# Performance work log

Measured on AMD Instinct MI355X. Metric: run time of the kernel, lower is better.

## Reference

```python
import jax, jax.numpy as jnp
import numpy as np

B, S, D, H, L = 4, 2048, 512, 8, 4
DFF = 4 * D
CW = 128          # context_window
LS_MIN, LS_MAX = -6.0, 1.5


def setup_inputs() -> dict:
    key = jax.random.key(0)
    ks = jax.random.split(key, 10)
    s = 0.02
    p = lambda k, shape: jax.random.normal(k, shape, jnp.float32) * s
    return {
        "x": jax.random.normal(ks[0], (B, S, 2), jnp.float32),
        "W_in": p(ks[1], (D, 2)), "b_in": jnp.zeros((D,), jnp.float32),
        "pos": p(ks[2], (1, S, D)),
        "Wqkv": p(ks[3], (L, 3 * D, D)), "bqkv": jnp.zeros((L, 3 * D), jnp.float32),
        "Wo": p(ks[4], (L, D, D)), "bo": jnp.zeros((L, D), jnp.float32),
        "W1": p(ks[5], (L, DFF, D)), "b1": jnp.zeros((L, DFF), jnp.float32),
        "W2": p(ks[6], (L, D, DFF)), "b2": jnp.zeros((L, D), jnp.float32),
        "ln1_g": jnp.ones((L, D), jnp.float32), "ln1_b": jnp.zeros((L, D), jnp.float32),
        "ln2_g": jnp.ones((L, D), jnp.float32), "ln2_b": jnp.zeros((L, D), jnp.float32),
        "W_head": p(ks[7], (4, D)), "b_head": jnp.zeros((4,), jnp.float32),
    }


def _ln(x, g, b):
    m = x.mean(-1, keepdims=True)
    v = ((x - m) ** 2).mean(-1, keepdims=True)
    return (x - m) / jnp.sqrt(v + 1e-5) * g + b


def reference(x, W_in, b_in, pos, Wqkv, bqkv, Wo, bo, W1, b1, W2, b2,
              ln1_g, ln1_b, ln2_g, ln2_b, W_head, b_head):
    Bx, Sx, _ = x.shape
    h = x @ W_in.T + b_in + pos[:, :Sx, :]          # [B,S,D]
    idx = jnp.arange(Sx)
    # True = disallowed: future OR older than context window
    mask = (idx[None, :] > idx[:, None]) | (idx[None, :] < idx[:, None] - CW)
    dh = D // H
    scale = 1.0 / np.sqrt(dh).astype(np.float32)
    neg = jnp.float32(-1e30)
    for l in range(L):
        # self-attention (post-LN, as nn.TransformerEncoderLayer default)
        qkv = h @ Wqkv[l].T + bqkv[l]               # [B,S,3D]
        q, k, v = jnp.split(qkv, 3, axis=-1)
        q = q.reshape(Bx, Sx, H, dh)
        k = k.reshape(Bx, Sx, H, dh)
        v = v.reshape(Bx, Sx, H, dh)
        scores = jnp.einsum('bqhd,bkhd->bhqk', q, k) * scale
        scores = jnp.where(mask, neg, scores)
        attn = jax.nn.softmax(scores, axis=-1)
        o = jnp.einsum('bhqk,bkhd->bqhd', attn, v).reshape(Bx, Sx, D)
        h = _ln(h + o @ Wo[l].T + bo[l], ln1_g[l], ln1_b[l])
        # GELU FFN (exact erf gelu, torch default)
        ff = jax.nn.gelu(h @ W1[l].T + b1[l], approximate=False) @ W2[l].T + b2[l]
        h = _ln(h + ff, ln2_g[l], ln2_b[l])
    out = h @ W_head.T + b_head                     # [B,S,4]
    mu = out[..., :2]
    log_sigma = jnp.clip(out[..., 2:], LS_MIN, LS_MAX)
    return mu, log_sigma
```

## Files before the change

kernel.cpp:

```cpp
#include <hip/hip_runtime.h>
#include <hip/hip_bf16.h>
#include <math.h>

constexpr int Bc = 4;
constexpr int Sc = 2048;
constexpr int Dc = 512;
constexpr int Hc = 8;
constexpr int DHc = 64;
constexpr int Lc = 4;
constexpr int DFFc = 2048;
constexpr int Tc = Bc * Sc;
constexpr int QKVW = 3 * Dc;

typedef __attribute__((ext_vector_type(8))) short short8;
typedef __attribute__((ext_vector_type(4))) float f32x4;
typedef __attribute__((ext_vector_type(4))) float float4v;
typedef __attribute__((ext_vector_type(4))) unsigned int uint4v;

static __device__ __forceinline__ float u16tof(unsigned int u) {
  return __uint_as_float(u << 16);
}
static __device__ __forceinline__ unsigned short ftobf(float f) {
  __hip_bfloat16 h = __float2bfloat16(f);
  return *reinterpret_cast<unsigned short*>(&h);
}
static __device__ __forceinline__ void gload_lds16(const void* g, void* l) {
  __builtin_amdgcn_global_load_lds(
      (const __attribute__((address_space(1))) void*)g,
      (__attribute__((address_space(3))) void*)l, 16, 0, 0);
}

static __device__ __forceinline__ int swzK(int row, int col) {
  return row * 64 + ((((col >> 3) ^ (row & 7)) << 3) | (col & 7));
}
static __device__ __forceinline__ int swzW(int row, int col) {
  return row * 192 + ((((col >> 3) ^ (row & 7)) << 3) | (col & 7));
}

__global__ __launch_bounds__(256) void k_f2bf(const float* __restrict__ in,
                                              unsigned short* __restrict__ out,
                                              int n) {
  int i = blockIdx.x * 256 + threadIdx.x;
  if (i < n) out[i] = ftobf(in[i]);
}

__global__ __launch_bounds__(256) void k_embed(const float* __restrict__ x,
                                               const float* __restrict__ W_in,
                                               const float* __restrict__ b_in,
                                               const float* __restrict__ pos,
                                               float* __restrict__ h,
                                               unsigned short* __restrict__ hb) {
  int idx = blockIdx.x * 256 + threadIdx.x;
  int t = idx >> 9;
  int d = idx & 511;
  int s = t & (Sc - 1);
  float v = x[t * 2 + 0] * W_in[d * 2 + 0] + x[t * 2 + 1] * W_in[d * 2 + 1] +
            b_in[d] + pos[(size_t)s * Dc + d];
  h[idx] = v;
  hb[idx] = ftobf(v);
}

template <int MODE, int OUTBF>
__global__ __launch_bounds__(256, 4) void k_mgemm(const unsigned short* __restrict__ A,
                                                  const unsigned short* __restrict__ W,
                                                  const float* __restrict__ bias,
                                                  void* __restrict__ Cout,
                                                  int M, int N, int K) {
  __shared__ short SMEM[2][2][512 * 8];
  const int tid = threadIdx.x;
  const int lane = tid & 63;
  const int wid = tid >> 6;
  const int wm = wid >> 1;
  const int wn = wid & 1;

  const int nwg = gridDim.x * gridDim.y;
  const int bid = blockIdx.y * gridDim.x + blockIdx.x;
  const int swz = (bid & 7) * (nwg >> 3) + (bid >> 3);
  const int m0 = (swz / gridDim.x) * 128;
  const int n0 = (swz % gridDim.x) * 128;

  int r0S, c0S, r1S, c1S;
  {
    int p = tid;
    int rp = p >> 3, q = (p & 7) ^ (rp & 7);
    r0S = (rp << 1) | (q >> 2);
    c0S = q & 3;
    p = tid + 256;
    rp = p >> 3;
    q = (p & 7) ^ (rp & 7);
    r1S = (rp << 1) | (q >> 2);
    c1S = q & 3;
  }
  const unsigned short* a0p = A + (size_t)(m0 + r0S) * K + c0S * 8;
  const unsigned short* a1p = A + (size_t)(m0 + r1S) * K + c1S * 8;
  const unsigned short* b0p = W + (size_t)(n0 + r0S) * K + c0S * 8;
  const unsigned short* b1p = W + (size_t)(n0 + r1S) * K + c1S * 8;
  const int d0 = (tid & ~63) * 8;
  const int d1 = ((tid + 256) & ~63) * 8;

  f32x4 acc[4][4] = {};
  const int lr = lane & 15;
  const int chr = lane >> 4;

  gload_lds16(a0p, &SMEM[0][0][d0]);
  gload_lds16(a1p, &SMEM[0][0][d1]);
  gload_lds16(b0p, &SMEM[1][0][d0]);
  gload_lds16(b1p, &SMEM[1][0][d1]);
  __syncthreads();

  const int nsteps = K >> 5;
  int buf = 0;
  for (int s = 0; s < nsteps; ++s) {
    if (s + 1 < nsteps) {
      const int ko = (s + 1) << 5;
      gload_lds16(a0p + ko, &SMEM[0][buf ^ 1][d0]);
      gload_lds16(a1p + ko, &SMEM[0][buf ^ 1][d1]);
      gload_lds16(b0p + ko, &SMEM[1][buf ^ 1][d0]);
      gload_lds16(b1p + ko, &SMEM[1][buf ^ 1][d1]);
    }
    short8 af[4], bfr[4];
#pragma unroll
    for (int mi = 0; mi < 4; ++mi) {
      int row = wm * 64 + mi * 16 + lr;
      int rp = row >> 1;
      int p = rp * 8 + (((((row & 1) << 2) | chr)) ^ (rp & 7));
      af[mi] = *(const short8*)&SMEM[0][buf][p * 8];
    }
#pragma unroll
    for (int ni = 0; ni < 4; ++ni) {
      int row = wn * 64 + ni * 16 + lr;
      int rp = row >> 1;
      int p = rp * 8 + (((((row & 1) << 2) | chr)) ^ (rp & 7));
      bfr[ni] = *(const short8*)&SMEM[1][buf][p * 8];
    }
#pragma unroll
    for (int mi = 0; mi < 4; ++mi)
#pragma unroll
      for (int ni = 0; ni < 4; ++ni)
        acc[mi][ni] = __builtin_amdgcn_mfma_f32_16x16x32_bf16(
            af[mi], bfr[ni], acc[mi][ni], 0, 0, 0);
    __syncthreads();
    buf ^= 1;
  }

  float* cw = (float*)&SMEM[0][0][0] + wid * (16 * 68);
  const int cj = lane & 15;
  const int rj4 = (lane >> 4) * 4;
  const int rrd = lane >> 3;
  const int crd = (lane & 7) * 8;
#pragma unroll
  for (int mi = 0; mi < 4; ++mi) {
#pragma unroll
    for (int ni = 0; ni < 4; ++ni) {
      float bn = bias[n0 + wn * 64 + ni * 16 + cj];
#pragma unroll
      for (int j = 0; j < 4; ++j) {
        float v = acc[mi][ni][j] + bn;
        if (MODE == 2) v = 0.5f * v * (1.0f + erff(v * 0.70710678118654752f));
        cw[(rj4 + j) * 68 + ni * 16 + cj] = v;
      }
    }
    __builtin_amdgcn_sched_barrier(0);
#pragma unroll
    for (int t = 0; t < 2; ++t) {
      int rl = t * 8 + rrd;
      float4v v0 = *(const float4v*)&cw[rl * 68 + crd];
      float4v v1 = *(const float4v*)&cw[rl * 68 + crd + 4];
      size_t gbase = (size_t)(m0 + wm * 64 + mi * 16 + rl) * N +
                     (n0 + wn * 64 + crd);
      if (OUTBF) {
        unsigned int w0 = ftobf(v0[0]) | ((unsigned int)ftobf(v0[1]) << 16);
        unsigned int w1 = ftobf(v0[2]) | ((unsigned int)ftobf(v0[3]) << 16);
        unsigned int w2 = ftobf(v1[0]) | ((unsigned int)ftobf(v1[1]) << 16);
        unsigned int w3 = ftobf(v1[2]) | ((unsigned int)ftobf(v1[3]) << 16);
        uint4v pk = {w0, w1, w2, w3};
        *(uint4v*)&((unsigned short*)Cout)[gbase] = pk;
      } else {
        *(float4v*)&((float*)Cout)[gbase] = v0;
        *(float4v*)&((float*)Cout)[gbase + 4] = v1;
      }
    }
    __builtin_amdgcn_sched_barrier(0);
  }
}

__global__ __launch_bounds__(256, 3) void k_attn(const unsigned short* __restrict__ qkv,
                                                 unsigned short* __restrict__ o) {
  __shared__ unsigned short KPs[192 * 64];
  __shared__ unsigned short Vt[64 * 192];

  const int tid = threadIdx.x;
  const int lane = tid & 63;
  const int w = tid >> 6;
  const int idx = blockIdx.x;
  const int qb = idx & 31;
  const int hh = (idx >> 5) & 7;
  const int b = idx >> 8;
  const int q0 = qb * 64;
  const int kstart = max(0, q0 - 128);
  const int nk = q0 + 64 - kstart;

  for (int c = tid; c < nk * 8; c += 256) {
    int j = c >> 3, ch = c & 7;
    short8 kv = *(const short8*)&qkv[(size_t)(b * Sc + kstart + j) * QKVW + Dc + hh * DHc + ch * 8];
    *(short8*)&KPs[swzK(j, ch * 8)] = kv;
  }
  for (int c = tid; c < (nk >> 1) * 8; c += 256) {
    int jp = c >> 3, ch = c & 7;
    int j = jp * 2;
    const unsigned short* base =
        &qkv[(size_t)(b * Sc + kstart + j) * QKVW + 2 * Dc + hh * DHc + ch * 8];
    short8 v0 = *(const short8*)base;
    short8 v1 = *(const short8*)(base + QKVW);
#pragma unroll
    for (int i = 0; i < 8; ++i) {
      unsigned int pk = (unsigned short)v0[i] | ((unsigned int)(unsigned short)v1[i] << 16);
      *(unsigned int*)&Vt[swzW(ch * 8 + i, j)] = pk;
    }
  }
  if (nk < 192) {
    for (int c = tid; c < 64 * 64; c += 256) {
      int d = c >> 6, jo = c & 63;
      *(unsigned int*)&Vt[swzW(d, 64 + jo * 2)] = 0;
    }
  }

  const int qg = q0 + w * 16 + (lane & 15);
  const int kg8 = (lane >> 4) * 8;
  const unsigned short* qp = &qkv[(size_t)(b * Sc + qg) * QKVW + hh * DHc + kg8];
  short8 bq0 = *(const short8*)qp;
  short8 bq1 = *(const short8*)(qp + 32);
  __syncthreads();

  const int jb = max(0, q0 + w * 16 - 128) - kstart;

  f32x4 sacc[9];
#pragma unroll
  for (int t = 0; t < 9; ++t) {
    int key = jb + t * 16 + (lane & 15);
    short8 a0 = *(const short8*)&KPs[swzK(key, kg8)];
    short8 a1 = *(const short8*)&KPs[swzK(key, 32 + kg8)];
    f32x4 z = {0.f, 0.f, 0.f, 0.f};
    z = __builtin_amdgcn_mfma_f32_16x16x32_bf16(a0, bq0, z, 0, 0, 0);
    sacc[t] = __builtin_amdgcn_mfma_f32_16x16x32_bf16(a1, bq1, z, 0, 0, 0);
  }

  const int rj = (lane >> 4) * 4;
  float mx = -1e30f;
#pragma unroll
  for (int t = 0; t < 9; ++t) {
#pragma unroll
    for (int j = 0; j < 4; ++j) {
      int kglob = kstart + jb + t * 16 + rj + j;
      bool valid = (kglob <= qg) && (kglob + 128 >= qg);
      float s = valid ? sacc[t][j] * 0.125f : -1e30f;
      sacc[t][j] = s;
      mx = fmaxf(mx, s);
    }
  }
  mx = fmaxf(mx, __shfl_xor(mx, 16));
  mx = fmaxf(mx, __shfl_xor(mx, 32));
  float sum = 0.f;
#pragma unroll
  for (int t = 0; t < 9; ++t)
#pragma unroll
    for (int j = 0; j < 4; ++j) {
      float e = __expf(sacc[t][j] - mx);
      sacc[t][j] = e;
      sum += e;
    }
  sum += __shfl_xor(sum, 16);
  sum += __shfl_xor(sum, 32);
  const float inv = 1.0f / sum;

  __syncthreads();

  const int prow = w * 16 + (lane & 15);
#pragma unroll
  for (int t = 0; t < 9; ++t) {
    int c0 = jb + t * 16 + rj;
    unsigned int p0 = ftobf(sacc[t][0] * inv) |
                      ((unsigned int)ftobf(sacc[t][1] * inv) << 16);
    unsigned int p1 = ftobf(sacc[t][2] * inv) |
                      ((unsigned int)ftobf(sacc[t][3] * inv) << 16);
    *(unsigned int*)&KPs[swzW(prow, c0)] = p0;
    *(unsigned int*)&KPs[swzW(prow, c0 + 2)] = p1;
  }
  {
    int g2 = (lane >> 4) * 2;
    for (int col = g2; col < jb; col += 8)
      *(unsigned int*)&KPs[swzW(prow, col)] = 0;
    for (int col = jb + 144 + g2; col < 192; col += 8)
      *(unsigned int*)&KPs[swzW(prow, col)] = 0;
  }
  f32x4 oacc[4] = {};
#pragma unroll
  for (int kb = 0; kb < 6; ++kb) {
    short8 pa = *(const short8*)&KPs[swzW(prow, kb * 32 + kg8)];
#pragma unroll
    for (int dt = 0; dt < 4; ++dt) {
      short8 vb = *(const short8*)&Vt[swzW(dt * 16 + (lane & 15), kb * 32 + kg8)];
      oacc[dt] = __builtin_amdgcn_mfma_f32_16x16x32_bf16(pa, vb, oacc[dt], 0, 0, 0);
    }
  }
  const int cj = lane & 15;
#pragma unroll
  for (int j = 0; j < 4; ++j)
#pragma unroll
    for (int dt = 0; dt < 4; ++dt)
      o[(size_t)(b * Sc + q0 + w * 16 + rj + j) * Dc + hh * DHc + dt * 16 + cj] =
          ftobf(oacc[dt][j]);
}

__global__ __launch_bounds__(256) void k_lnr(float* __restrict__ h,
                                             const float* __restrict__ raw,
                                             const float* __restrict__ g,
                                             const float* __restrict__ bta,
                                             unsigned short* __restrict__ outb) {
  const int wid = threadIdx.x >> 6;
  const int lane = threadIdx.x & 63;
  const int t = blockIdx.x * 4 + wid;
  const float4v* hrow = (const float4v*)(h + (size_t)t * Dc);
  const float4v* rrow = (const float4v*)(raw + (size_t)t * Dc);
  float4v v[2];
  float sum = 0.0f, sq = 0.0f;
#pragma unroll
  for (int i = 0; i < 2; ++i) {
    float4v hv = hrow[lane + i * 64];
    float4v rv = rrow[lane + i * 64];
#pragma unroll
    for (int c = 0; c < 4; ++c) {
      float xv = rv[c] + hv[c];
      v[i][c] = xv;
      sum += xv;
      sq += xv * xv;
    }
  }
#pragma unroll
  for (int off = 32; off; off >>= 1) {
    sum += __shfl_xor(sum, off);
    sq += __shfl_xor(sq, off);
  }
  float m = sum * (1.0f / 512.0f);
  float var = sq * (1.0f / 512.0f) - m * m;
  float rstd = rsqrtf(var + 1e-5f);
  float4v* orow = (float4v*)(h + (size_t)t * Dc);
  unsigned int* brow = (unsigned int*)(outb + (size_t)t * Dc);
#pragma unroll
  for (int i = 0; i < 2; ++i) {
    int d4 = (lane + i * 64) * 4;
    float4v ov;
#pragma unroll
    for (int c = 0; c < 4; ++c)
      ov[c] = (v[i][c] - m) * rstd * g[d4 + c] + bta[d4 + c];
    orow[lane + i * 64] = ov;
    unsigned int p0 = ftobf(ov[0]) | ((unsigned int)ftobf(ov[1]) << 16);
    unsigned int p1 = ftobf(ov[2]) | ((unsigned int)ftobf(ov[3]) << 16);
    brow[(lane + i * 64) * 2] = p0;
    brow[(lane + i * 64) * 2 + 1] = p1;
  }
}

__global__ __launch_bounds__(256) void k_head(const float* __restrict__ h,
                                              const float* __restrict__ Wh,
                                              const float* __restrict__ bh,
                                              float* __restrict__ outp) {
  const int wid = threadIdx.x >> 6;
  const int lane = threadIdx.x & 63;
  const int t = blockIdx.x * 4 + wid;
  const float* row = h + (size_t)t * Dc;
  float a0 = 0, a1 = 0, a2 = 0, a3 = 0;
#pragma unroll
  for (int i = 0; i < 8; ++i) {
    int d = lane + i * 64;
    float xv = row[d];
    a0 += xv * Wh[0 * Dc + d];
    a1 += xv * Wh[1 * Dc + d];
    a2 += xv * Wh[2 * Dc + d];
    a3 += xv * Wh[3 * Dc + d];
  }
#pragma unroll
  for (int off = 32; off; off >>= 1) {
    a0 += __shfl_xor(a0, off);
    a1 += __shfl_xor(a1, off);
    a2 += __shfl_xor(a2, off);
    a3 += __shfl_xor(a3, off);
  }
  if (lane == 0) {
    outp[(size_t)t * 2 + 0] = a0 + bh[0];
    outp[(size_t)t * 2 + 1] = a1 + bh[1];
    outp[(size_t)Tc * 2 + (size_t)t * 2 + 0] = fminf(fmaxf(a2 + bh[2], -6.0f), 1.5f);
    outp[(size_t)Tc * 2 + (size_t)t * 2 + 1] = fminf(fmaxf(a3 + bh[3], -6.0f), 1.5f);
  }
}

extern "C" void kernel_launch(void* const* d_in, const int* in_sizes, int n_in,
                              void* d_out, int out_size, void* d_ws, size_t ws_size,
                              hipStream_t stream) {
  const float* x    = (const float*)d_in[0];
  const float* W_in = (const float*)d_in[1];
  const float* b_in = (const float*)d_in[2];
  const float* pos  = (const float*)d_in[3];
  const float* Wqkv = (const float*)d_in[4];
  const float* bqkv = (const float*)d_in[5];
  const float* Wo   = (const float*)d_in[6];
  const float* bo   = (const float*)d_in[7];
  const float* W1   = (const float*)d_in[8];
  const float* b1   = (const float*)d_in[9];
  const float* W2   = (const float*)d_in[10];
  const float* b2   = (const float*)d_in[11];
  const float* ln1g = (const float*)d_in[12];
  const float* ln1b = (const float*)d_in[13];
  const float* ln2g = (const float*)d_in[14];
  const float* ln2b = (const float*)d_in[15];
  const float* Wh   = (const float*)d_in[16];
  const float* bh   = (const float*)d_in[17];
  float* out = (float*)d_out;

  char* p = (char*)d_ws;
  float* h   = (float*)p;          p += (size_t)Tc * Dc * 4;
  float* t2  = (float*)p;          p += (size_t)Tc * Dc * 4;
  unsigned short* hb  = (unsigned short*)p; p += (size_t)Tc * Dc * 2;
  unsigned short* ob  = (unsigned short*)p; p += (size_t)Tc * Dc * 2;
  unsigned short* big = (unsigned short*)p; p += (size_t)Tc * DFFc * 2;
  unsigned short* wqb = (unsigned short*)p; p += (size_t)Lc * QKVW * Dc * 2;
  unsigned short* wob = (unsigned short*)p; p += (size_t)Lc * Dc * Dc * 2;
  unsigned short* w1b = (unsigned short*)p; p += (size_t)Lc * DFFc * Dc * 2;
  unsigned short* w2b = (unsigned short*)p; p += (size_t)Lc * Dc * DFFc * 2;

  k_f2bf<<<Lc * QKVW * Dc / 256, 256, 0, stream>>>(Wqkv, wqb, Lc * QKVW * Dc);
  k_f2bf<<<Lc * Dc * Dc / 256, 256, 0, stream>>>(Wo, wob, Lc * Dc * Dc);
  k_f2bf<<<Lc * DFFc * Dc / 256, 256, 0, stream>>>(W1, w1b, Lc * DFFc * Dc);
  k_f2bf<<<Lc * Dc * DFFc / 256, 256, 0, stream>>>(W2, w2b, Lc * Dc * DFFc);

  k_embed<<<(Tc * Dc) / 256, 256, 0, stream>>>(x, W_in, b_in, pos, h, hb);

  for (int l = 0; l < Lc; ++l) {
    const unsigned short* wq_l = wqb + (size_t)l * QKVW * Dc;
    const unsigned short* wo_l = wob + (size_t)l * Dc * Dc;
    const unsigned short* w1_l = w1b + (size_t)l * DFFc * Dc;
    const unsigned short* w2_l = w2b + (size_t)l * Dc * DFFc;

    k_mgemm<0, 1><<<dim3(QKVW / 128, Tc / 128), 256, 0, stream>>>(
        hb, wq_l, bqkv + (size_t)l * QKVW, big, Tc, QKVW, Dc);

    k_attn<<<Bc * Hc * (Sc / 64), 256, 0, stream>>>(big, ob);

    k_mgemm<0, 0><<<dim3(Dc / 128, Tc / 128), 256, 0, stream>>>(
        ob, wo_l, bo + (size_t)l * Dc, t2, Tc, Dc, Dc);

    k_lnr<<<Tc / 4, 256, 0, stream>>>(h, t2, ln1g + (size_t)l * Dc,
                                      ln1b + (size_t)l * Dc, hb);

    k_mgemm<2, 1><<<dim3(DFFc / 128, Tc / 128), 256, 0, stream>>>(
        hb, w1_l, b1 + (size_t)l * DFFc, big, Tc, DFFc, Dc);

    k_mgemm<0, 0><<<dim3(Dc / 128, Tc / 128), 256, 0, stream>>>(
        big, w2_l, b2 + (size_t)l * Dc, t2, Tc, Dc, DFFc);

    k_lnr<<<Tc / 4, 256, 0, stream>>>(h, t2, ln2g + (size_t)l * Dc,
                                      ln2b + (size_t)l * Dc, hb);
  }

  k_head<<<Tc / 4, 256, 0, stream>>>(h, Wh, bh, out);
}
```

Baseline: 606.0 us.

## Fuse weight conversions into one vectorized kernel, vectorize embed, trim attention PV loop

The four fp32-to-bf16 weight conversion launches become a single kernel that processes four elements per thread with 16-byte loads and 8-byte stores. The embedding kernel is vectorized the same way. The attention PV loop now covers only the key blocks that overlap the valid window, skipping MFMAs over blocks that are all zero. The GEMM fragment-index computation is moved into a helper with no change in behavior. Together these cut launch overhead, memory transactions and wasted MFMA work, at the cost of a runtime-bounded loop in attention that is no longer fully unrolled.

```diff
diff --git a/kernel.cpp b/kernel.cpp
--- a/kernel.cpp
+++ b/kernel.cpp
@@ -16,6 +16,7 @@
 typedef __attribute__((ext_vector_type(4))) float f32x4;
 typedef __attribute__((ext_vector_type(4))) float float4v;
 typedef __attribute__((ext_vector_type(4))) unsigned int uint4v;
+typedef __attribute__((ext_vector_type(2))) unsigned int uint2v;
 
 static __device__ __forceinline__ float u16tof(unsigned int u) {
   return __uint_as_float(u << 16);
@@ -36,12 +37,32 @@
 static __device__ __forceinline__ int swzW(int row, int col) {
   return row * 192 + ((((col >> 3) ^ (row & 7)) << 3) | (col & 7));
 }
-
-__global__ __launch_bounds__(256) void k_f2bf(const float* __restrict__ in,
-                                              unsigned short* __restrict__ out,
-                                              int n) {
-  int i = blockIdx.x * 256 + threadIdx.x;
-  if (i < n) out[i] = ftobf(in[i]);
+static __device__ __forceinline__ int gperm(int row, int ch) {
+  return (row >> 1) * 8 + (((((row & 1) << 2) | ch)) ^ ((row >> 1) & 7));
+}
+
+__global__ __launch_bounds__(256) void k_f2bf4(const float* __restrict__ p0,
+                                               const float* __restrict__ p1,
+                                               const float* __restrict__ p2,
+                                               const float* __restrict__ p3,
+                                               unsigned short* __restrict__ o0,
+                                               unsigned short* __restrict__ o1,
+                                               unsigned short* __restrict__ o2,
+                                               unsigned short* __restrict__ o3,
+                                               int n0, int n01, int n012, int n0123) {
+  int i4 = (blockIdx.x * 256 + threadIdx.x) * 4;
+  if (i4 >= n0123) return;
+  const float* src;
+  unsigned short* dst;
+  int off;
+  if (i4 < n0) { src = p0; dst = o0; off = i4; }
+  else if (i4 < n01) { src = p1; dst = o1; off = i4 - n0; }
+  else if (i4 < n012) { src = p2; dst = o2; off = i4 - n01; }
+  else { src = p3; dst = o3; off = i4 - n012; }
+  float4v v = *(const float4v*)&src[off];
+  uint2v pk = {ftobf(v[0]) | ((unsigned int)ftobf(v[1]) << 16),
+               ftobf(v[2]) | ((unsigned int)ftobf(v[3]) << 16)};
+  *(uint2v*)&dst[off] = pk;
 }
 
 __global__ __launch_bounds__(256) void k_embed(const float* __restrict__ x,
@@ -50,14 +71,24 @@
                                                const float* __restrict__ pos,
                                                float* __restrict__ h,
                                                unsigned short* __restrict__ hb) {
-  int idx = blockIdx.x * 256 + threadIdx.x;
-  int t = idx >> 9;
-  int d = idx & 511;
+  int i4 = (blockIdx.x * 256 + threadIdx.x) * 4;
+  int t = i4 >> 9;
+  int d = i4 & 511;
   int s = t & (Sc - 1);
-  float v = x[t * 2 + 0] * W_in[d * 2 + 0] + x[t * 2 + 1] * W_in[d * 2 + 1] +
-            b_in[d] + pos[(size_t)s * Dc + d];
-  h[idx] = v;
-  hb[idx] = ftobf(v);
+  float x0 = x[t * 2 + 0], x1 = x[t * 2 + 1];
+  float4v w01 = *(const float4v*)&W_in[d * 2];
+  float4v w23 = *(const float4v*)&W_in[d * 2 + 4];
+  float4v pz = *(const float4v*)&pos[(size_t)s * Dc + d];
+  float4v b4 = *(const float4v*)&b_in[d];
+  float4v v;
+  v[0] = x0 * w01[0] + x1 * w01[1] + b4[0] + pz[0];
+  v[1] = x0 * w01[2] + x1 * w01[3] + b4[1] + pz[1];
+  v[2] = x0 * w23[0] + x1 * w23[1] + b4[2] + pz[2];
+  v[3] = x0 * w23[2] + x1 * w23[3] + b4[3] + pz[3];
+  *(float4v*)&h[i4] = v;
+  uint2v pk = {ftobf(v[0]) | ((unsigned int)ftobf(v[1]) << 16),
+               ftobf(v[2]) | ((unsigned int)ftobf(v[3]) << 16)};
+  *(uint2v*)&hb[i4] = pk;
 }
 
 template <int MODE, int OUTBF>
@@ -120,19 +151,11 @@
     }
     short8 af[4], bfr[4];
 #pragma unroll
-    for (int mi = 0; mi < 4; ++mi) {
-      int row = wm * 64 + mi * 16 + lr;
-      int rp = row >> 1;
-      int p = rp * 8 + (((((row & 1) << 2) | chr)) ^ (rp & 7));
-      af[mi] = *(const short8*)&SMEM[0][buf][p * 8];
-    }
-#pragma unroll
-    for (int ni = 0; ni < 4; ++ni) {
-      int row = wn * 64 + ni * 16 + lr;
-      int rp = row >> 1;
-      int p = rp * 8 + (((((row & 1) << 2) | chr)) ^ (rp & 7));
-      bfr[ni] = *(const short8*)&SMEM[1][buf][p * 8];
-    }
+    for (int mi = 0; mi < 4; ++mi)
+      af[mi] = *(const short8*)&SMEM[0][buf][gperm(wm * 64 + mi * 16 + lr, chr) * 8];
+#pragma unroll
+    for (int ni = 0; ni < 4; ++ni)
+      bfr[ni] = *(const short8*)&SMEM[1][buf][gperm(wn * 64 + ni * 16 + lr, chr) * 8];
 #pragma unroll
     for (int mi = 0; mi < 4; ++mi)
 #pragma unroll
@@ -293,9 +316,10 @@
     for (int col = jb + 144 + g2; col < 192; col += 8)
       *(unsigned int*)&KPs[swzW(prow, col)] = 0;
   }
+  const int kb0 = jb >> 5;
+  const int kbend = min(6, (jb + 144 + 31) >> 5);
   f32x4 oacc[4] = {};
-#pragma unroll
-  for (int kb = 0; kb < 6; ++kb) {
+  for (int kb = kb0; kb < kbend; ++kb) {
     short8 pa = *(const short8*)&KPs[swzW(prow, kb * 32 + kg8)];
 #pragma unroll
     for (int dt = 0; dt < 4; ++dt) {
@@ -428,12 +452,15 @@
   unsigned short* w1b = (unsigned short*)p; p += (size_t)Lc * DFFc * Dc * 2;
   unsigned short* w2b = (unsigned short*)p; p += (size_t)Lc * Dc * DFFc * 2;
 
-  k_f2bf<<<Lc * QKVW * Dc / 256, 256, 0, stream>>>(Wqkv, wqb, Lc * QKVW * Dc);
-  k_f2bf<<<Lc * Dc * Dc / 256, 256, 0, stream>>>(Wo, wob, Lc * Dc * Dc);
-  k_f2bf<<<Lc * DFFc * Dc / 256, 256, 0, stream>>>(W1, w1b, Lc * DFFc * Dc);
-  k_f2bf<<<Lc * Dc * DFFc / 256, 256, 0, stream>>>(W2, w2b, Lc * Dc * DFFc);
-
-  k_embed<<<(Tc * Dc) / 256, 256, 0, stream>>>(x, W_in, b_in, pos, h, hb);
+  const int nq = Lc * QKVW * Dc;
+  const int no = Lc * Dc * Dc;
+  const int n1 = Lc * DFFc * Dc;
+  const int n2 = Lc * Dc * DFFc;
+  const int ntot = nq + no + n1 + n2;
+  k_f2bf4<<<ntot / 1024, 256, 0, stream>>>(Wqkv, Wo, W1, W2, wqb, wob, w1b, w2b,
+                                           nq, nq + no, nq + no + n1, ntot);
+
+  k_embed<<<(Tc * Dc) / 1024, 256, 0, stream>>>(x, W_in, b_in, pos, h, hb);
 
   for (int l = 0; l < Lc; ++l) {
     const unsigned short* wq_l = wqb + (size_t)l * QKVW * Dc;
```

New measurement: 592.4 us. 2.3% less time.
